# Performance work log

Hardware: AMD Instinct MI355X
Metric: run time of the kernel (lower is better)

The kernel has to match this reference:

```python
import jax, jax.numpy as jnp
import numpy as np

B, IMG, C = 128, 128, 3
NP = 8                      # n_patches per side
PS = IMG // NP              # patch size = 16
IN_D = C * PS * PS          # 768
E, NH, L, A = 768, 12, 12, 256
HS = E // NH                # 64
T = NP * NP + 1             # 65 tokens (cls + patches)
LN_EPS = 1e-5


def _pos_emb(seq_len, d):
    i = np.arange(seq_len, dtype=np.float64)[:, None]
    j = np.arange(d, dtype=np.float64)[None, :]
    even = np.sin(i / 10000 ** (j / d))
    odd = np.cos(i / 10000 ** ((j - 1) / d))
    return jnp.asarray(np.where(j % 2 == 0, even, odd), dtype=jnp.float32)


def setup_inputs() -> dict:
    key = jax.random.key(0)
    ks = jax.random.split(key, 16)
    s_e = 1.0 / np.sqrt(E)
    s_in = 1.0 / np.sqrt(IN_D)
    s_4e = 1.0 / np.sqrt(4 * E)
    return {
        "images": jax.random.normal(ks[0], (B, IMG, IMG, C), jnp.float32),
        "lin_w": jax.random.normal(ks[1], (IN_D, E), jnp.float32) * s_in,
        "cls_tok": jax.random.uniform(ks[2], (1, E), jnp.float32),
        "pos_emb": _pos_emb(T, E),
        "Wq": jax.random.normal(ks[3], (L, E, E), jnp.float32) * s_e,
        "Wk": jax.random.normal(ks[4], (L, E, E), jnp.float32) * s_e,
        "Wv": jax.random.normal(ks[5], (L, E, E), jnp.float32) * s_e,
        "Wo": jax.random.normal(ks[6], (L, E, E), jnp.float32) * s_e,
        "bo": jnp.zeros((L, E), jnp.float32),
        "ln1g": jnp.ones((L, E), jnp.float32),
        "ln1b": jnp.zeros((L, E), jnp.float32),
        "ln2g": jnp.ones((L, E), jnp.float32),
        "ln2b": jnp.zeros((L, E), jnp.float32),
        "W1": jax.random.normal(ks[7], (L, E, 4 * E), jnp.float32) * s_e,
        "b1": jnp.zeros((L, 4 * E), jnp.float32),
        "W2": jax.random.normal(ks[8], (L, 4 * E, E), jnp.float32) * s_4e,
        "b2": jnp.zeros((L, E), jnp.float32),
        "head_w": jax.random.normal(ks[9], (E, A), jnp.float32) * s_e,
        "head_b": jnp.zeros((A,), jnp.float32),
    }


def _layernorm(x, g, b):
    mu = jnp.mean(x, axis=-1, keepdims=True)
    var = jnp.var(x, axis=-1, keepdims=True)
    return (x - mu) * jax.lax.rsqrt(var + LN_EPS) * g + b


def _vit_forward(images, lin_w, cls_tok, pos_emb, Wq, Wk, Wv, Wo, bo,
                 ln1g, ln1b, ln2g, ln2b, W1, b1, W2, b2, head_w, head_b):
    n = images.shape[0]
    # patches: 'b (h p1) (w p2) c -> b (h w) (p1 p2 c)'
    p = images.reshape(n, NP, PS, NP, PS, C)
    patches = p.transpose(0, 1, 3, 2, 4, 5).reshape(n, NP * NP, IN_D)
    x = patches @ lin_w                                   # [B, 64, E]
    x = jnp.concatenate([jnp.broadcast_to(cls_tok, (n, 1, E)), x], axis=1)
    x = x + pos_emb[None]                                 # [B, T, E]

    scale = E ** (-0.5)  # NOTE: original scales by n_embd, not head_size

    def block(x, params):
        wq, wk, wv, wo_, bo_, g1, be1, g2, be2, w1, bb1, w2, bb2 = params
        h = _layernorm(x, g1, be1)
        q = (h @ wq).reshape(n, T, NH, HS)
        k = (h @ wk).reshape(n, T, NH, HS)
        v = (h @ wv).reshape(n, T, NH, HS)
        wei = jnp.einsum('bthd,bshd->bhts', q, k) * scale
        wei = jax.nn.softmax(wei, axis=-1)
        attn = jnp.einsum('bhts,bshd->bthd', wei, v).reshape(n, T, E)
        x = x + attn @ wo_ + bo_
        h2 = _layernorm(x, g2, be2)
        x = x + jax.nn.relu(h2 @ w1 + bb1) @ w2 + bb2
        return x, None

    x, _ = jax.lax.scan(block, x,
                        (Wq, Wk, Wv, Wo, bo, ln1g, ln1b, ln2g, ln2b,
                         W1, b1, W2, b2))
    cls = x[:, 0]                                          # [B, E]
    logits = jax.nn.softmax(cls @ head_w + head_b, axis=-1)  # model ends in Softmax
    return logits


def reference(images, lin_w, cls_tok, pos_emb, Wq, Wk, Wv, Wo, bo,
              ln1g, ln1b, ln2g, ln2b, W1, b1, W2, b2, head_w, head_b):
    return _vit_forward(images, lin_w, cls_tok, pos_emb, Wq, Wk, Wv, Wo, bo,
                        ln1g, ln1b, ln2g, ln2b, W1, b1, W2, b2, head_w, head_b)
```

## Files before the change

### kernel.cpp

```cpp
#include <hip/hip_runtime.h>
#include <cstdint>
#include <cstddef>


typedef __bf16 bf16x8 __attribute__((ext_vector_type(8)));
typedef float  f32x4  __attribute__((ext_vector_type(4)));

#define DEVINL __device__ __forceinline__

DEVINL uint16_t f2bf(float f){
  union U{float f; uint32_t i;} v; v.f=f; uint32_t u=v.i;
  return (uint16_t)((u + 0x7fffu + ((u>>16)&1u)) >> 16);
}

DEVINL void gl_lds16(const void* g, void* l){
  __builtin_amdgcn_global_load_lds((const __attribute__((address_space(1))) void*)g,
                                   (__attribute__((address_space(3))) void*)l, 16, 0, 0);
}

__global__ __launch_bounds__(256) void patchify_k(const float* __restrict__ img,
                                                  uint16_t* __restrict__ out){
  int i = blockIdx.x*256 + threadIdx.x;
  int m  = i / 768, kk = i - m*768;
  int b  = m >> 6,  t  = m & 63;
  int py = t >> 3,  px = t & 7;
  int r  = kk / 48, rem = kk - r*48;
  size_t src = ((size_t)(b*128 + py*16 + r)*128 + px*16)*3 + rem;
  out[i] = f2bf(img[src]);
}

DEVINL void tile_transpose(const float* __restrict__ src, uint16_t* __restrict__ dst,
                           int R, int C, int ti, int tj, int tid){
  __shared__ uint16_t tile[32][33];
  int tx = tid & 31, ty = tid >> 5;
  int r0 = ti*32, c0 = tj*32;
  #pragma unroll
  for (int i=0;i<4;++i)
    tile[ty+i*8][tx] = f2bf(src[(size_t)(r0+ty+i*8)*C + c0 + tx]);
  __syncthreads();
  #pragma unroll
  for (int i=0;i<4;++i)
    dst[(size_t)(c0+ty+i*8)*R + r0 + tx] = tile[tx][ty+i*8];
}

__global__ __launch_bounds__(256) void transpose_cvt_k(const float* __restrict__ src,
                                                       uint16_t* __restrict__ dst, int R, int C){
  tile_transpose(src, dst, R, C, blockIdx.y, blockIdx.x, threadIdx.x);
}

__global__ __launch_bounds__(256) void prep_layer_k(
    const float* __restrict__ Wq, const float* __restrict__ Wk,
    const float* __restrict__ Wv, const float* __restrict__ Wo,
    const float* __restrict__ W1, const float* __restrict__ W2,
    uint16_t* __restrict__ wbuf){
  int idx = blockIdx.x;
  const float* src; uint16_t* dst; int R, C, ti, tj;
  if (idx < 2304){
    int m = idx / 576, t = idx - m*576; ti = t/24; tj = t - ti*24; R=768; C=768;
    src = (m==0)?Wq:(m==1)?Wk:(m==2)?Wv:Wo;
    dst = wbuf + (size_t)m*589824;
  } else if (idx < 4608){
    int t = idx - 2304; ti = t/96; tj = t - ti*96; R=768; C=3072;
    src = W1; dst = wbuf + 2359296;
  } else {
    int t = idx - 4608; ti = t/24; tj = t - ti*24; R=3072; C=768;
    src = W2; dst = wbuf + 4718592;
  }
  tile_transpose(src, dst, R, C, ti, tj, threadIdx.x);
}

__global__ __launch_bounds__(256) void cls_init_k(const float* __restrict__ ct,
                                                  const float* __restrict__ pos,
                                                  float* __restrict__ X){
  int b = blockIdx.x, tid = threadIdx.x;
  for (int e = tid; e < 768; e += 256)
    X[(size_t)b*65*768 + e] = ct[e] + pos[e];
}

template<int MODE>
__global__ __launch_bounds__(256) void ln_k(const float* __restrict__ Xin,
                                            float* __restrict__ Xout,
                                            const float* __restrict__ P1,
                                            const float* __restrict__ bias2,
                                            uint16_t* __restrict__ H,
                                            const float* __restrict__ g,
                                            const float* __restrict__ b){
  int row = blockIdx.x, tid = threadIdx.x;
  const size_t ro = (size_t)row*768;
  const float* xr = Xin + ro;
  float v0, v1, v2;
  if constexpr (MODE==1){
    const float* p1 = P1 + ro;
    v0 = xr[tid]     + p1[tid];
    v1 = xr[tid+256] + p1[tid+256];
    v2 = xr[tid+512] + p1[tid+512];
    float* xo = Xout + ro;
    xo[tid] = v0; xo[tid+256] = v1; xo[tid+512] = v2;
  } else if constexpr (MODE==2){
    const float* p1 = P1 + ro;
    v0 = xr[tid]     + p1[tid]     + bias2[tid];
    v1 = xr[tid+256] + p1[tid+256] + bias2[tid+256];
    v2 = xr[tid+512] + p1[tid+512] + bias2[tid+512];
    float* xo = Xout + ro;
    xo[tid] = v0; xo[tid+256] = v1; xo[tid+512] = v2;
  } else {
    v0 = xr[tid]; v1 = xr[tid+256]; v2 = xr[tid+512];
  }
  int wid = tid>>6, lane = tid&63;
  __shared__ float part[4];
  __shared__ float bc[2];
  float s = v0+v1+v2;
  #pragma unroll
  for (int o=32;o;o>>=1) s += __shfl_down(s,o);
  if (lane==0) part[wid] = s;
  __syncthreads();
  if (tid==0) bc[0] = (part[0]+part[1]+part[2]+part[3]) * (1.f/768.f);
  __syncthreads();
  float mu = bc[0];
  float d0=v0-mu, d1=v1-mu, d2=v2-mu;
  float q = d0*d0 + d1*d1 + d2*d2;
  #pragma unroll
  for (int o=32;o;o>>=1) q += __shfl_down(q,o);
  __syncthreads();
  if (lane==0) part[wid] = q;
  __syncthreads();
  if (tid==0) bc[1] = rsqrtf((part[0]+part[1]+part[2]+part[3])*(1.f/768.f) + 1e-5f);
  __syncthreads();
  float rs = bc[1];
  uint16_t* hr = H + ro;
  hr[tid]     = f2bf(d0*rs*g[tid]     + b[tid]);
  hr[tid+256] = f2bf(d1*rs*g[tid+256] + b[tid+256]);
  hr[tid+512] = f2bf(d2*rs*g[tid+512] + b[tid+512]);
}

enum { EP_BF16=0, EP_RES=1, EP_RELU=2, EP_EMB=3, EP_OUTF32=4 };

template<int MODE, int BN>
__global__ __launch_bounds__(256) void gemm_bt_k(
    const uint16_t* __restrict__ A, const uint16_t* __restrict__ Bt,
    int M, int N, int K, int strideB, long long strideO,
    const float* __restrict__ bias, float* __restrict__ X,
    uint16_t* __restrict__ Obf, const float* __restrict__ pos,
    float* __restrict__ Pout)
{
  constexpr int WN = BN/2;
  constexpr int NF = WN/16;
  constexpr int BLOADS = BN/64;
  __shared__ __align__(16) uint16_t sA[3][128*32];
  __shared__ __align__(16) uint16_t sB[3][BN*32];
  const int tid = threadIdx.x;
  const int wid = tid>>6, lane = tid&63;
  const int nx = gridDim.x;
  const int nwg = nx*gridDim.y;
  int idx = blockIdx.y*nx + blockIdx.x;
  int q8 = nwg>>3, r8 = nwg&7, xcd = idx&7, off = idx>>3;
  int swz = (xcd<r8 ? xcd*(q8+1) : r8*(q8+1) + (xcd-r8)*q8) + off;
  const int bn = (swz % nx)*BN, bm = (swz / nx)*128;
  const int z = blockIdx.z;
  const uint16_t* Bz = Bt + (size_t)z*strideB;
  const int wr = wid>>1, wc = wid&1;
  const int frow = lane&15, g = lane>>4;
  int srA[2], scA[2];
  #pragma unroll
  for (int rr=0; rr<2; ++rr){
    int G = rr*256 + tid;
    srA[rr] = G>>2; scA[rr] = ((G&3) - (G>>3)) & 3;
  }
  int srB[BLOADS], scB[BLOADS];
  #pragma unroll
  for (int rr=0; rr<BLOADS; ++rr){
    int G = rr*256 + tid;
    srB[rr] = G>>2; scB[rr] = ((G&3) - (G>>3)) & 3;
  }
  const int rsw = (frow>>1)&3;
  f32x4 acc[4][NF] = {};
  const int nt = K>>5;

  auto stage = [&](char* dA, char* dB, int k0){
    #pragma unroll
    for (int rr=0; rr<2; ++rr)
      gl_lds16(A + (size_t)(bm+srA[rr])*K + k0 + scA[rr]*8, dA + (rr*256 + wid*64)*16);
    #pragma unroll
    for (int rr=0; rr<BLOADS; ++rr)
      gl_lds16(Bz + (size_t)(bn+srB[rr])*K + k0 + scB[rr]*8, dB + (rr*256 + wid*64)*16);
  };

  char *cA=(char*)sA[0], *nA=(char*)sA[1], *fA=(char*)sA[2];
  char *cB=(char*)sB[0], *nB=(char*)sB[1], *fB=(char*)sB[2];
  stage(cA, cB, 0);
  stage(nA, nB, 32);

  for (int t = 0; t < nt; ++t){
    if (t+2 < nt){
      stage(fA, fB, (t+2)<<5);
      if constexpr (BLOADS==1) asm volatile("s_waitcnt vmcnt(6)" ::: "memory");
      else                     asm volatile("s_waitcnt vmcnt(8)" ::: "memory");
    } else if (t+1 < nt){
      if constexpr (BLOADS==1) asm volatile("s_waitcnt vmcnt(3)" ::: "memory");
      else                     asm volatile("s_waitcnt vmcnt(4)" ::: "memory");
    } else {
      asm volatile("s_waitcnt vmcnt(0)" ::: "memory");
    }
    __builtin_amdgcn_s_barrier();
    bf16x8 a[4], b[NF];
    #pragma unroll
    for (int m=0;m<4;++m)
      a[m] = *(const bf16x8*)(cA + (wr*64+m*16+frow)*64 + (((g+rsw)&3)<<4));
    #pragma unroll
    for (int n=0;n<NF;++n)
      b[n] = *(const bf16x8*)(cB + (wc*WN+n*16+frow)*64 + (((g+rsw)&3)<<4));
    #pragma unroll
    for (int m=0;m<4;++m)
      #pragma unroll
      for (int n=0;n<NF;++n)
        acc[m][n] = __builtin_amdgcn_mfma_f32_16x16x32_bf16(a[m], b[n], acc[m][n], 0,0,0);
    __builtin_amdgcn_s_barrier();
    char* t1=cA; cA=nA; nA=fA; fA=t1;
    char* t2=cB; cB=nB; nB=fB; fB=t2;
  }

  uint16_t* Oz = Obf ? Obf + (size_t)z*(size_t)strideO : nullptr;
  #pragma unroll
  for (int m=0;m<4;++m){
    int gr0 = bm + wr*64 + m*16 + (lane>>4)*4;
    #pragma unroll
    for (int n=0;n<NF;++n){
      int gc = bn + wc*WN + n*16 + (lane&15);
      #pragma unroll
      for (int r=0;r<4;++r){
        int grow = gr0 + r;
        float vsum = acc[m][n][r];
        if constexpr (MODE==EP_BF16){
          Oz[(size_t)grow*N + gc] = f2bf(vsum);
        } else if constexpr (MODE==EP_RES){
          X[(size_t)grow*N + gc] += vsum + bias[gc];
        } else if constexpr (MODE==EP_RELU){
          float u = vsum + bias[gc];
          Oz[(size_t)grow*N + gc] = f2bf(u > 0.f ? u : 0.f);
        } else if constexpr (MODE==EP_OUTF32){
          Pout[(size_t)grow*N + gc] = vsum;
        } else {
          int t2i = grow & 63, bb = grow >> 6;
          X[((size_t)bb*65 + 1 + t2i)*768 + gc] = vsum + pos[(size_t)(t2i+1)*768 + gc];
        }
      }
    }
  }
}

template<int MODE, int SK>
__global__ __launch_bounds__(512) void gemm2m_k(
    const uint16_t* __restrict__ A, const uint16_t* __restrict__ Bt,
    int M, int N, int K, int strideB, long long strideO,
    const float* __restrict__ bias, float* __restrict__ X,
    uint16_t* __restrict__ Obf, float* __restrict__ P1)
{
  __shared__ __align__(16) uint16_t sA[2][256*32];
  __shared__ __align__(16) uint16_t sB[2][128*32];
  const int tid = threadIdx.x;
  const int wid = tid>>6, lane = tid&63;
  const int nx = gridDim.x;
  const int nwg = nx*gridDim.y;
  int idx = blockIdx.y*nx + blockIdx.x;
  int q8 = nwg>>3, r8 = nwg&7, xcd = idx&7, off = idx>>3;
  int swz = (xcd<r8 ? xcd*(q8+1) : r8*(q8+1) + (xcd-r8)*q8) + off;
  const int bn = (swz % nx)*128, bm = (swz / nx)*256;
  const int z = blockIdx.z;
  const uint16_t* Bz = (SK==1) ? Bt + (size_t)z*strideB : Bt;
  const int kbase = (SK==1) ? 0 : z*(K/SK);
  const int KS = (SK==1) ? K : K/SK;
  const int wr = wid>>1, wc = wid&1;
  const int frow = lane&15, g = lane>>4;
  int srA[2], scA[2];
  #pragma unroll
  for (int rr=0; rr<2; ++rr){
    int G = rr*512 + tid;
    srA[rr] = G>>2; scA[rr] = ((G&3) - (G>>3)) & 3;
  }
  const int srB = tid>>2, scB = ((tid&3) - (tid>>3)) & 3;
  const int rsw = (frow>>1)&3;
  f32x4 acc[4][4] = {};
  const int nt = KS>>5;

  auto stage = [&](int bsel, int k0){
    char* dA = (char*)sA[bsel]; char* dB = (char*)sB[bsel];
    #pragma unroll
    for (int rr=0; rr<2; ++rr)
      gl_lds16(A + (size_t)(bm+srA[rr])*K + kbase + k0 + scA[rr]*8,
               dA + (rr*512 + wid*64)*16);
    gl_lds16(Bz + (size_t)(bn+srB)*K + kbase + k0 + scB*8, dB + (wid*64)*16);
  };

  stage(0, 0);
  int buf = 0;
  for (int t = 0; t < nt; ++t){
    if (t+1 < nt){
      stage(buf^1, (t+1)<<5);
      asm volatile("s_waitcnt vmcnt(3)" ::: "memory");
    } else {
      asm volatile("s_waitcnt vmcnt(0)" ::: "memory");
    }
    __builtin_amdgcn_s_barrier();
    const char* sAc = (const char*)sA[buf];
    const char* sBc = (const char*)sB[buf];
    bf16x8 a[4], b[4];
    #pragma unroll
    for (int m=0;m<4;++m)
      a[m] = *(const bf16x8*)(sAc + (wr*64+m*16+frow)*64 + (((g+rsw)&3)<<4));
    #pragma unroll
    for (int n=0;n<4;++n)
      b[n] = *(const bf16x8*)(sBc + (wc*64+n*16+frow)*64 + (((g+rsw)&3)<<4));
    #pragma unroll
    for (int m=0;m<4;++m)
      #pragma unroll
      for (int n=0;n<4;++n)
        acc[m][n] = __builtin_amdgcn_mfma_f32_16x16x32_bf16(a[m], b[n], acc[m][n], 0,0,0);
    __builtin_amdgcn_s_barrier();
    buf ^= 1;
  }

  uint16_t* Oz = Obf ? Obf + (size_t)z*(size_t)strideO : nullptr;
  #pragma unroll
  for (int m=0;m<4;++m){
    int gr0 = bm + wr*64 + m*16 + (lane>>4)*4;
    #pragma unroll
    for (int n=0;n<4;++n){
      int gc = bn + wc*64 + n*16 + (lane&15);
      #pragma unroll
      for (int r=0;r<4;++r){
        int grow = gr0 + r;
        if (grow < M){
          float vsum = acc[m][n][r];
          if constexpr (MODE==EP_BF16){
            Oz[(size_t)grow*N + gc] = f2bf(vsum);
          } else if constexpr (MODE==EP_RES){
            if constexpr (SK==1){
              X[(size_t)grow*N + gc] += vsum + bias[gc];
            } else {
              if (z==0) X[(size_t)grow*N + gc] += vsum + bias[gc];
              else      P1[(size_t)grow*N + gc] = vsum;
            }
          } else if constexpr (MODE==EP_RELU){
            float u = vsum + bias[gc];
            Oz[(size_t)grow*N + gc] = f2bf(u > 0.f ? u : 0.f);
          }
        }
      }
    }
  }
}

__global__ __launch_bounds__(320) void attn_mfma_k(const uint16_t* __restrict__ q,
    const uint16_t* __restrict__ k, const uint16_t* __restrict__ v,
    uint16_t* __restrict__ o)
{
  __shared__ __align__(16) uint16_t P_lds[80][104];
  __shared__ __align__(16) uint16_t Vt[64][104];
  const int bh = blockIdx.x; const int b = bh / 12, hd = bh - b*12;
  const int tid = threadIdx.x;
  const int m = tid>>6;
  const int lane = tid&63;
  const int g = lane>>4, c = lane&15;
  const size_t base = (size_t)b*65*768 + (size_t)hd*64;

  for (int i = tid; i < 80*16; i += 320) P_lds[i>>4][80 + (i&15)] = 0;
  for (int i = tid; i < 64*32; i += 320) Vt[i>>5][64 + (i&31)] = 0;
  __syncthreads();
  for (int j = tid; j < 520; j += 320){
    int key = j >> 3, dc = j & 7;
    union { bf16x8 v8; uint16_t u[8]; } gv;
    gv.v8 = *(const bf16x8*)&v[base + (size_t)key*768 + dc*8];
    #pragma unroll
    for (int e = 0; e < 8; ++e) Vt[dc*8 + e][key] = gv.u[e];
  }

  bf16x8 bk[5][2];
  #pragma unroll
  for (int n=0;n<5;++n)
    #pragma unroll
    for (int kk=0;kk<2;++kk)
      bk[n][kk] = *(const bf16x8*)&k[base + (size_t)(n*16 + c)*768 + kk*32 + g*8];

  bf16x8 aq[2];
  #pragma unroll
  for (int kk=0;kk<2;++kk)
    aq[kk] = *(const bf16x8*)&q[base + (size_t)(m*16 + c)*768 + kk*32 + g*8];
  f32x4 sacc[5] = {};
  #pragma unroll
  for (int kk=0;kk<2;++kk)
    #pragma unroll
    for (int n=0;n<5;++n)
      sacc[n] = __builtin_amdgcn_mfma_f32_16x16x32_bf16(aq[kk], bk[n][kk], sacc[n], 0,0,0);

  const float scale = 0.03608439182435161f;
  #pragma unroll
  for (int r=0;r<4;++r){
    float val[5]; float mx = -3.0e38f;
    #pragma unroll
    for (int n=0;n<5;++n){
      val[n] = (n*16 + c) < 65 ? sacc[n][r]*scale : -3.0e38f;
      mx = fmaxf(mx, val[n]);
    }
    #pragma unroll
    for (int off=1; off<16; off<<=1) mx = fmaxf(mx, __shfl_xor(mx, off));
    float p[5], sum = 0.f;
    #pragma unroll
    for (int n=0;n<5;++n){
      p[n] = (n*16 + c) < 65 ? __expf(val[n]-mx) : 0.f;
      sum += p[n];
    }
    #pragma unroll
    for (int off=1; off<16; off<<=1) sum += __shfl_xor(sum, off);
    float rinv = 1.f / sum;
    int row = m*16 + g*4 + r;
    #pragma unroll
    for (int n=0;n<5;++n) P_lds[row][n*16 + c] = f2bf(p[n]*rinv);
  }
  __syncthreads();

  bf16x8 vb[4][3];
  #pragma unroll
  for (int n=0;n<4;++n)
    #pragma unroll
    for (int kk=0;kk<3;++kk)
      vb[n][kk] = *(const bf16x8*)&Vt[n*16 + c][kk*32 + g*8];
  f32x4 oacc[4] = {};
  #pragma unroll
  for (int kk=0;kk<3;++kk){
    bf16x8 pa = *(const bf16x8*)&P_lds[m*16 + c][kk*32 + g*8];
    #pragma unroll
    for (int n=0;n<4;++n)
      oacc[n] = __builtin_amdgcn_mfma_f32_16x16x32_bf16(pa, vb[n][kk], oacc[n], 0,0,0);
  }
  #pragma unroll
  for (int r=0;r<4;++r){
    int row = m*16 + g*4 + r;
    if (row < 65){
      #pragma unroll
      for (int n=0;n<4;++n)
        o[base + (size_t)row*768 + n*16 + c] = f2bf(oacc[n][r]);
    }
  }
}

__global__ __launch_bounds__(256) void head_k(const float* __restrict__ X,
    const float* __restrict__ P1,
    const float* __restrict__ W, const float* __restrict__ bias,
    float* __restrict__ out){
  int b = blockIdx.x, a = threadIdx.x;
  const size_t ro = (size_t)b*65*768;
  const float* xr = X + ro;
  const float* p1 = P1 + ro;
  float acc = bias[a];
  for (int kk=0; kk<768; ++kk)
    acc += (xr[kk]+p1[kk])*W[(size_t)kk*256 + a];
  int wid = a>>6, lane = a&63;
  __shared__ float red[4];
  float mx = acc;
  #pragma unroll
  for (int off=32; off; off>>=1) mx = fmaxf(mx, __shfl_xor(mx, off));
  if (lane==0) red[wid]=mx;
  __syncthreads();
  mx = fmaxf(fmaxf(red[0],red[1]), fmaxf(red[2],red[3]));
  float e = __expf(acc-mx);
  float s = e;
  #pragma unroll
  for (int off=32; off; off>>=1) s += __shfl_xor(s, off);
  __syncthreads();
  if (lane==0) red[wid]=s;
  __syncthreads();
  s = red[0]+red[1]+red[2]+red[3];
  out[(size_t)b*256 + a] = e/s;
}

extern "C" void kernel_launch(void* const* d_in, const int* in_sizes, int n_in,
                              void* d_out, int out_size, void* d_ws, size_t ws_size,
                              hipStream_t stream)
{
  const float* images = (const float*)d_in[0];
  const float* lin_w  = (const float*)d_in[1];
  const float* cls_tok= (const float*)d_in[2];
  const float* pos    = (const float*)d_in[3];
  const float* Wq = (const float*)d_in[4];
  const float* Wk = (const float*)d_in[5];
  const float* Wv = (const float*)d_in[6];
  const float* Wo = (const float*)d_in[7];
  const float* bo = (const float*)d_in[8];
  const float* ln1g=(const float*)d_in[9];
  const float* ln1b=(const float*)d_in[10];
  const float* ln2g=(const float*)d_in[11];
  const float* ln2b=(const float*)d_in[12];
  const float* W1 = (const float*)d_in[13];
  const float* b1 = (const float*)d_in[14];
  const float* W2 = (const float*)d_in[15];
  const float* b2 = (const float*)d_in[16];
  const float* hw = (const float*)d_in[17];
  const float* hb = (const float*)d_in[18];

  char* ws = (char*)d_ws;
  float*    x    = (float*)   (ws + 0);
  uint16_t* attn = (uint16_t*)(ws + 25559040);
  float*    P1   = (float*)   (ws + 25559040);
  uint16_t* qkv  = (uint16_t*)(ws + 38338560);
  uint16_t* h    = (uint16_t*)(ws + 76677120);
  uint16_t* mid  = (uint16_t*)(ws + 89456640);
  float*    woP  = (float*)   (ws + 89456640);
  uint16_t* wbuf = (uint16_t*)(ws + 140574720);
  uint16_t* lwt  = (uint16_t*)(ws + 154730496);

  patchify_k<<<24576,256,0,stream>>>(images, mid);
  transpose_cvt_k<<<dim3(24,24),256,0,stream>>>(lin_w, lwt, 768, 768);
  gemm_bt_k<EP_EMB,128><<<dim3(6,64,1),256,0,stream>>>(mid, lwt, 8192,768,768, 0,0,
                                                   nullptr, x, nullptr, pos, nullptr);
  cls_init_k<<<128,256,0,stream>>>(cls_tok, pos, x);

  for (int l=0;l<12;++l){
    prep_layer_k<<<6912,256,0,stream>>>(Wq+(size_t)l*589824, Wk+(size_t)l*589824,
                                        Wv+(size_t)l*589824, Wo+(size_t)l*589824,
                                        W1+(size_t)l*2359296, W2+(size_t)l*2359296, wbuf);
    if (l==0)
      ln_k<0><<<8320,256,0,stream>>>(x, nullptr, nullptr, nullptr, h, ln1g, ln1b);
    else
      ln_k<1><<<8320,256,0,stream>>>(x, x, P1, nullptr, h,
                                     ln1g+(size_t)l*768, ln1b+(size_t)l*768);
    gemm2m_k<EP_BF16,1><<<dim3(6,33,3),512,0,stream>>>(h, wbuf, 8320,768,768,
                                                       589824, 6389760LL,
                                                       nullptr, nullptr, qkv, nullptr);
    attn_mfma_k<<<1536,320,0,stream>>>(qkv, qkv+6389760, qkv+12779520, attn);
    gemm_bt_k<EP_OUTF32,128><<<dim3(6,65,1),256,0,stream>>>(attn, wbuf+1769472,
                                                     8320,768,768, 0,0,
                                                     nullptr, nullptr, nullptr, nullptr, woP);
    ln_k<2><<<8320,256,0,stream>>>(x, x, woP, bo+(size_t)l*768, h,
                                   ln2g+(size_t)l*768, ln2b+(size_t)l*768);
    gemm2m_k<EP_RELU,1><<<dim3(24,33,1),512,0,stream>>>(h, wbuf+2359296, 8320,3072,768,
                                                        0,0, b1+(size_t)l*3072, nullptr, mid, nullptr);
    gemm2m_k<EP_RES,2><<<dim3(6,33,2),512,0,stream>>>(mid, wbuf+4718592, 8320,768,3072,
                                                      0,0, b2+(size_t)l*768, x, nullptr, P1);
  }
  head_k<<<128,256,0,stream>>>(x, P1, hw, hb, (float*)d_out);
}
```

Before: 3.100 ms.

## Split-K the Wo and FFN-down GEMMs and restructure gemm_bt pipeline barriers

Splits the attention output projection into two K halves writing separate fp32 partials, and raises the FFN down-projection split-K from two to three slices with a new P2 buffer. The layernorm and head kernels now sum both partials. The gemm_bt main loop is reordered to issue the next prefetch before the MFMAs and to wait and barrier after compute. Both GEMM kernels also raise wave priority around the MFMA block. The intent is more workgroups on these small-N GEMMs to fill the GPU and better load/compute overlap. The cost is extra fp32 partial writes and reads.

```diff
diff --git a/kernel.cpp b/kernel.cpp
--- a/kernel.cpp
+++ b/kernel.cpp
@@ -80,7 +80,8 @@
 template<int MODE>
 __global__ __launch_bounds__(256) void ln_k(const float* __restrict__ Xin,
                                             float* __restrict__ Xout,
-                                            const float* __restrict__ P1,
+                                            const float* __restrict__ Pa,
+                                            const float* __restrict__ Pb,
                                             const float* __restrict__ bias2,
                                             uint16_t* __restrict__ H,
                                             const float* __restrict__ g,
@@ -90,17 +91,17 @@
   const float* xr = Xin + ro;
   float v0, v1, v2;
   if constexpr (MODE==1){
-    const float* p1 = P1 + ro;
-    v0 = xr[tid]     + p1[tid];
-    v1 = xr[tid+256] + p1[tid+256];
-    v2 = xr[tid+512] + p1[tid+512];
+    const float* p1 = Pa + ro; const float* p2 = Pb + ro;
+    v0 = xr[tid]     + p1[tid]     + p2[tid];
+    v1 = xr[tid+256] + p1[tid+256] + p2[tid+256];
+    v2 = xr[tid+512] + p1[tid+512] + p2[tid+512];
     float* xo = Xout + ro;
     xo[tid] = v0; xo[tid+256] = v1; xo[tid+512] = v2;
-  } else if constexpr (MODE==2){
-    const float* p1 = P1 + ro;
-    v0 = xr[tid]     + p1[tid]     + bias2[tid];
-    v1 = xr[tid+256] + p1[tid+256] + bias2[tid+256];
-    v2 = xr[tid+512] + p1[tid+512] + bias2[tid+512];
+  } else if constexpr (MODE==3){
+    const float* p1 = Pa + ro; const float* p2 = Pb + ro;
+    v0 = xr[tid]     + p1[tid]     + p2[tid]     + bias2[tid];
+    v1 = xr[tid+256] + p1[tid+256] + p2[tid+256] + bias2[tid+256];
+    v2 = xr[tid+512] + p1[tid+512] + p2[tid+512] + bias2[tid+512];
     float* xo = Xout + ro;
     xo[tid] = v0; xo[tid+256] = v1; xo[tid+512] = v2;
   } else {
@@ -135,7 +136,7 @@
 
 enum { EP_BF16=0, EP_RES=1, EP_RELU=2, EP_EMB=3, EP_OUTF32=4 };
 
-template<int MODE, int BN>
+template<int MODE, int BN, int SK>
 __global__ __launch_bounds__(256) void gemm_bt_k(
     const uint16_t* __restrict__ A, const uint16_t* __restrict__ Bt,
     int M, int N, int K, int strideB, long long strideO,
@@ -157,7 +158,9 @@
   int swz = (xcd<r8 ? xcd*(q8+1) : r8*(q8+1) + (xcd-r8)*q8) + off;
   const int bn = (swz % nx)*BN, bm = (swz / nx)*128;
   const int z = blockIdx.z;
-  const uint16_t* Bz = Bt + (size_t)z*strideB;
+  const uint16_t* Bz = (SK==1) ? Bt + (size_t)z*strideB : Bt;
+  const int kbase = (SK==1) ? 0 : z*(K/SK);
+  const int KS = (SK==1) ? K : K/SK;
   const int wr = wid>>1, wc = wid&1;
   const int frow = lane&15, g = lane>>4;
   int srA[2], scA[2];
@@ -174,34 +177,27 @@
   }
   const int rsw = (frow>>1)&3;
   f32x4 acc[4][NF] = {};
-  const int nt = K>>5;
+  const int nt = KS>>5;
 
   auto stage = [&](char* dA, char* dB, int k0){
     #pragma unroll
     for (int rr=0; rr<2; ++rr)
-      gl_lds16(A + (size_t)(bm+srA[rr])*K + k0 + scA[rr]*8, dA + (rr*256 + wid*64)*16);
+      gl_lds16(A + (size_t)(bm+srA[rr])*K + kbase + k0 + scA[rr]*8, dA + (rr*256 + wid*64)*16);
     #pragma unroll
     for (int rr=0; rr<BLOADS; ++rr)
-      gl_lds16(Bz + (size_t)(bn+srB[rr])*K + k0 + scB[rr]*8, dB + (rr*256 + wid*64)*16);
+      gl_lds16(Bz + (size_t)(bn+srB[rr])*K + kbase + k0 + scB[rr]*8, dB + (rr*256 + wid*64)*16);
   };
 
   char *cA=(char*)sA[0], *nA=(char*)sA[1], *fA=(char*)sA[2];
   char *cB=(char*)sB[0], *nB=(char*)sB[1], *fB=(char*)sB[2];
   stage(cA, cB, 0);
   stage(nA, nB, 32);
+  if constexpr (BLOADS==1) asm volatile("s_waitcnt vmcnt(3)" ::: "memory");
+  else                     asm volatile("s_waitcnt vmcnt(4)" ::: "memory");
+  __builtin_amdgcn_s_barrier();
 
   for (int t = 0; t < nt; ++t){
-    if (t+2 < nt){
-      stage(fA, fB, (t+2)<<5);
-      if constexpr (BLOADS==1) asm volatile("s_waitcnt vmcnt(6)" ::: "memory");
-      else                     asm volatile("s_waitcnt vmcnt(8)" ::: "memory");
-    } else if (t+1 < nt){
-      if constexpr (BLOADS==1) asm volatile("s_waitcnt vmcnt(3)" ::: "memory");
-      else                     asm volatile("s_waitcnt vmcnt(4)" ::: "memory");
-    } else {
-      asm volatile("s_waitcnt vmcnt(0)" ::: "memory");
-    }
-    __builtin_amdgcn_s_barrier();
+    if (t+2 < nt) stage(fA, fB, (t+2)<<5);
     bf16x8 a[4], b[NF];
     #pragma unroll
     for (int m=0;m<4;++m)
@@ -209,17 +205,28 @@
     #pragma unroll
     for (int n=0;n<NF;++n)
       b[n] = *(const bf16x8*)(cB + (wc*WN+n*16+frow)*64 + (((g+rsw)&3)<<4));
+    __builtin_amdgcn_s_setprio(1);
     #pragma unroll
     for (int m=0;m<4;++m)
       #pragma unroll
       for (int n=0;n<NF;++n)
         acc[m][n] = __builtin_amdgcn_mfma_f32_16x16x32_bf16(a[m], b[n], acc[m][n], 0,0,0);
-    __builtin_amdgcn_s_barrier();
+    __builtin_amdgcn_s_setprio(0);
+    if (t+1 < nt){
+      if (t+2 < nt){
+        if constexpr (BLOADS==1) asm volatile("s_waitcnt vmcnt(3)" ::: "memory");
+        else                     asm volatile("s_waitcnt vmcnt(4)" ::: "memory");
+      } else {
+        asm volatile("s_waitcnt vmcnt(0)" ::: "memory");
+      }
+      __builtin_amdgcn_s_barrier();
+    }
     char* t1=cA; cA=nA; nA=fA; fA=t1;
     char* t2=cB; cB=nB; nB=fB; fB=t2;
   }
 
   uint16_t* Oz = Obf ? Obf + (size_t)z*(size_t)strideO : nullptr;
+  float* Pz = Pout ? Pout + (size_t)z*(size_t)M*N : nullptr;
   #pragma unroll
   for (int m=0;m<4;++m){
     int gr0 = bm + wr*64 + m*16 + (lane>>4)*4;
@@ -238,7 +245,7 @@
           float u = vsum + bias[gc];
           Oz[(size_t)grow*N + gc] = f2bf(u > 0.f ? u : 0.f);
         } else if constexpr (MODE==EP_OUTF32){
-          Pout[(size_t)grow*N + gc] = vsum;
+          Pz[(size_t)grow*N + gc] = vsum;
         } else {
           int t2i = grow & 63, bb = grow >> 6;
           X[((size_t)bb*65 + 1 + t2i)*768 + gc] = vsum + pos[(size_t)(t2i+1)*768 + gc];
@@ -253,7 +260,7 @@
     const uint16_t* __restrict__ A, const uint16_t* __restrict__ Bt,
     int M, int N, int K, int strideB, long long strideO,
     const float* __restrict__ bias, float* __restrict__ X,
-    uint16_t* __restrict__ Obf, float* __restrict__ P1)
+    uint16_t* __restrict__ Obf, float* __restrict__ P1, float* __restrict__ P2)
 {
   __shared__ __align__(16) uint16_t sA[2][256*32];
   __shared__ __align__(16) uint16_t sB[2][128*32];
@@ -310,11 +317,13 @@
     #pragma unroll
     for (int n=0;n<4;++n)
       b[n] = *(const bf16x8*)(sBc + (wc*64+n*16+frow)*64 + (((g+rsw)&3)<<4));
+    __builtin_amdgcn_s_setprio(1);
     #pragma unroll
     for (int m=0;m<4;++m)
       #pragma unroll
       for (int n=0;n<4;++n)
         acc[m][n] = __builtin_amdgcn_mfma_f32_16x16x32_bf16(a[m], b[n], acc[m][n], 0,0,0);
+    __builtin_amdgcn_s_setprio(0);
     __builtin_amdgcn_s_barrier();
     buf ^= 1;
   }
@@ -337,8 +346,9 @@
             if constexpr (SK==1){
               X[(size_t)grow*N + gc] += vsum + bias[gc];
             } else {
-              if (z==0) X[(size_t)grow*N + gc] += vsum + bias[gc];
-              else      P1[(size_t)grow*N + gc] = vsum;
+              if (z==0)      X[(size_t)grow*N + gc] += vsum + bias[gc];
+              else if (z==1) P1[(size_t)grow*N + gc] = vsum;
+              else           P2[(size_t)grow*N + gc] = vsum;
             }
           } else if constexpr (MODE==EP_RELU){
             float u = vsum + bias[gc];
@@ -444,16 +454,17 @@
 }
 
 __global__ __launch_bounds__(256) void head_k(const float* __restrict__ X,
-    const float* __restrict__ P1,
+    const float* __restrict__ P1, const float* __restrict__ P2,
     const float* __restrict__ W, const float* __restrict__ bias,
     float* __restrict__ out){
   int b = blockIdx.x, a = threadIdx.x;
   const size_t ro = (size_t)b*65*768;
   const float* xr = X + ro;
   const float* p1 = P1 + ro;
+  const float* p2 = P2 + ro;
   float acc = bias[a];
   for (int kk=0; kk<768; ++kk)
-    acc += (xr[kk]+p1[kk])*W[(size_t)kk*256 + a];
+    acc += (xr[kk]+p1[kk]+p2[kk])*W[(size_t)kk*256 + a];
   int wid = a>>6, lane = a&63;
   __shared__ float red[4];
   float mx = acc;
@@ -502,6 +513,7 @@
   uint16_t* attn = (uint16_t*)(ws + 25559040);
   float*    P1   = (float*)   (ws + 25559040);
   uint16_t* qkv  = (uint16_t*)(ws + 38338560);
+  float*    P2   = (float*)   (ws + 51118080);
   uint16_t* h    = (uint16_t*)(ws + 76677120);
   uint16_t* mid  = (uint16_t*)(ws + 89456640);
   float*    woP  = (float*)   (ws + 89456640);
@@ -510,7 +522,7 @@
 
   patchify_k<<<24576,256,0,stream>>>(images, mid);
   transpose_cvt_k<<<dim3(24,24),256,0,stream>>>(lin_w, lwt, 768, 768);
-  gemm_bt_k<EP_EMB,128><<<dim3(6,64,1),256,0,stream>>>(mid, lwt, 8192,768,768, 0,0,
+  gemm_bt_k<EP_EMB,128,1><<<dim3(6,64,1),256,0,stream>>>(mid, lwt, 8192,768,768, 0,0,
                                                    nullptr, x, nullptr, pos, nullptr);
   cls_init_k<<<128,256,0,stream>>>(cls_tok, pos, x);
 
@@ -519,23 +531,23 @@
                                         Wv+(size_t)l*589824, Wo+(size_t)l*589824,
                                         W1+(size_t)l*2359296, W2+(size_t)l*2359296, wbuf);
     if (l==0)
-      ln_k<0><<<8320,256,0,stream>>>(x, nullptr, nullptr, nullptr, h, ln1g, ln1b);
+      ln_k<0><<<8320,256,0,stream>>>(x, nullptr, nullptr, nullptr, nullptr, h, ln1g, ln1b);
     else
-      ln_k<1><<<8320,256,0,stream>>>(x, x, P1, nullptr, h,
+      ln_k<1><<<8320,256,0,stream>>>(x, x, P1, P2, nullptr, h,
                                      ln1g+(size_t)l*768, ln1b+(size_t)l*768);
     gemm2m_k<EP_BF16,1><<<dim3(6,33,3),512,0,stream>>>(h, wbuf, 8320,768,768,
                                                        589824, 6389760LL,
-                                                       nullptr, nullptr, qkv, nullptr);
+                                                       nullptr, nullptr, qkv, nullptr, nullptr);
     attn_mfma_k<<<1536,320,0,stream>>>(qkv, qkv+6389760, qkv+12779520, attn);
-    gemm_bt_k<EP_OUTF32,128><<<dim3(6,65,1),256,0,stream>>>(attn, wbuf+1769472,
+    gemm_bt_k<EP_OUTF32,128,2><<<dim3(6,65,2),256,0,stream>>>(attn, wbuf+1769472,
                                                      8320,768,768, 0,0,
                                                      nullptr, nullptr, nullptr, nullptr, woP);
-    ln_k<2><<<8320,256,0,stream>>>(x, x, woP, bo+(size_t)l*768, h,
+    ln_k<3><<<8320,256,0,stream>>>(x, x, woP, woP+6389760, bo+(size_t)l*768, h,
                                    ln2g+(size_t)l*768, ln2b+(size_t)l*768);
     gemm2m_k<EP_RELU,1><<<dim3(24,33,1),512,0,stream>>>(h, wbuf+2359296, 8320,3072,768,
-                                                        0,0, b1+(size_t)l*3072, nullptr, mid, nullptr);
-    gemm2m_k<EP_RES,2><<<dim3(6,33,2),512,0,stream>>>(mid, wbuf+4718592, 8320,768,3072,
-                                                      0,0, b2+(size_t)l*768, x, nullptr, P1);
-  }
-  head_k<<<128,256,0,stream>>>(x, P1, hw, hb, (float*)d_out);
-}
+                                                        0,0, b1+(size_t)l*3072, nullptr, mid, nullptr, nullptr);
+    gemm2m_k<EP_RES,3><<<dim3(6,33,3),512,0,stream>>>(mid, wbuf+4718592, 8320,768,3072,
+                                                      0,0, b2+(size_t)l*768, x, nullptr, P1, P2);
+  }
+  head_k<<<128,256,0,stream>>>(x, P1, P2, hw, hb, (float*)d_out);
+}
```

Result: slower. 3.368 ms (+8.7%).
